# Kernel tuning notes

Hardware: AMD Instinct MI355X
Metric: run time of the kernel (lower is better)

The kernel has to match this reference:

```python
import jax, jax.numpy as jnp
import numpy as np

NUM_HEADS = 16

def setup_inputs() -> dict:
    key = jax.random.key(0)
    ks = jax.random.split(key, 9)
    B, S, D = 2, 2048, 1024
    scale = 1.0 / np.sqrt(D)
    x = jax.random.normal(ks[0], (B, S, D), dtype=jnp.float32)
    def lin(k):
        kw, kb = jax.random.split(k)
        w = jax.random.uniform(kw, (D, D), jnp.float32, -scale, scale)
        b = jax.random.uniform(kb, (D,), jnp.float32, -scale, scale)
        return w, b
    wq, bq = lin(ks[1])
    wk, bk = lin(ks[2])
    wv, bv = lin(ks[3])
    wo, bo = lin(ks[4])
    return {"x": x, "wq": wq, "bq": bq, "wk": wk, "bk": bk,
            "wv": wv, "bv": bv, "wo": wo, "bo": bo}

def reference(x, wq, bq, wk, bk, wv, bv, wo, bo):
    # Prefill path: past_kv=None, use_cache=False, dropout in eval mode (identity).
    B, S, D = x.shape
    H = NUM_HEADS
    Hd = D // H
    # Linear layers: y = x @ W^T + b (torch nn.Linear convention)
    q = (x @ wq.T + bq).reshape(B, S, H, Hd)
    k = (x @ wk.T + bk).reshape(B, S, H, Hd)
    v = (x @ wv.T + bv).reshape(B, S, H, Hd)
    # scores: (B, H, S, S)
    scores = jnp.einsum("bqhd,bkhd->bhqk", q, k) / np.sqrt(Hd).astype(np.float32)
    # causal mask (seq_len > 1 and past_kv is None)
    causal = jnp.tril(jnp.ones((S, S), dtype=bool))
    scores = jnp.where(causal, scores, -jnp.inf)
    probs = jax.nn.softmax(scores, axis=-1)
    attn = jnp.einsum("bhqk,bkhd->bqhd", probs, v).reshape(B, S, D)
    return attn @ wo.T + bo
```

## Files before the change

kernel.cpp:

```cpp
#include <hip/hip_runtime.h>
#include <hip/hip_bf16.h>
#include <math.h>

constexpr int Bt   = 2;
constexpr int Sseq = 2048;
constexpr int Dm   = 1024;
constexpr int Hh   = 16;
constexpr int Mrows = Bt * Sseq;
constexpr int Kd    = 1024;

typedef __attribute__((ext_vector_type(8))) short bf16x8;
typedef __attribute__((ext_vector_type(4))) float f32x4;

__device__ __forceinline__ ushort bfhi(float x) {
    __hip_bfloat16 h = __float2bfloat16(x);
    return *reinterpret_cast<ushort*>(&h);
}
__device__ __forceinline__ float bf2f(ushort u) {
    __hip_bfloat16 h;
    *reinterpret_cast<ushort*>(&h) = u;
    return __bfloat162float(h);
}
__device__ __forceinline__ void split2(float x, ushort& h, ushort& l) {
    h = bfhi(x);
    l = bfhi(x - bf2f(h));
}

template<int MODE>
__global__ __launch_bounds__(256)
void gemm_bf16x2(const float* __restrict__ A,
                 const float* __restrict__ W0, const float* __restrict__ W1,
                 const float* __restrict__ W2,
                 const float* __restrict__ b0, const float* __restrict__ b1,
                 const float* __restrict__ b2,
                 float* __restrict__ Cf,
                 ushort* __restrict__ qk_hi, ushort* __restrict__ qk_lo,
                 ushort* __restrict__ vt_hi, ushort* __restrict__ vt_lo)
{
    __shared__ alignas(16) ushort As[128 * 64];
    __shared__ alignas(16) ushort Bs[128 * 64];

    const int tid = threadIdx.x, lane = tid & 63, w = tid >> 6;

    const int gx = gridDim.x;
    int bid = blockIdx.y * gx + blockIdx.x;
    int cpx = (gx * gridDim.y) >> 3;
    int sb  = (bid & 7) * cpx + (bid >> 3);
    const int m0 = (sb / gx) * 128;
    const int j0 = (sb % gx) * 128;

    const int wsel = j0 >> 10;
    const float* __restrict__ W    = (wsel == 0) ? W0 : ((wsel == 1) ? W1 : W2);
    const float* __restrict__ bias = (wsel == 0) ? b0 : ((wsel == 1) ? b1 : b2);
    const int jj0 = j0 & 1023;

    const int wr = w >> 1, wc = w & 1;
    const int rl = lane & 15, kq = lane >> 4;
    const int sw0 = rl & 7;

    const int srow  = tid >> 1;
    const int khalf = tid & 1;
    const int rsw   = srow & 7;

    const float* ga0 = A + (size_t)(m0  + srow) * Kd + khalf * 16;
    const float* gb0 = W + (size_t)(jj0 + srow) * Kd + khalf * 16;

    f32x4 acc[4][4] = {};
    float av[16], bv[16];

    #pragma unroll
    for (int p = 0; p < 4; ++p) {
        *(float4*)&av[p * 4] = *(const float4*)(ga0 + p * 4);
        *(float4*)&bv[p * 4] = *(const float4*)(gb0 + p * 4);
    }

    for (int k0 = 0; k0 < Kd; k0 += 32) {
        __syncthreads();
        {
            ushort* pa = As + srow * 64;
            ushort* pb = Bs + srow * 64;
            #pragma unroll
            for (int t = 0; t < 2; ++t) {
                bf16x8 hia, loa, hib, lob;
                #pragma unroll
                for (int e = 0; e < 8; ++e) {
                    float xa = av[t * 8 + e], xb = bv[t * 8 + e];
                    ushort ha, la, hb, lb;
                    split2(xa, ha, la); split2(xb, hb, lb);
                    hia[e] = (short)ha; loa[e] = (short)la;
                    hib[e] = (short)hb; lob[e] = (short)lb;
                }
                int s = khalf * 2 + t;
                *(bf16x8*)(pa + ((s    ) ^ rsw) * 8) = hia;
                *(bf16x8*)(pa + ((s + 4) ^ rsw) * 8) = loa;
                *(bf16x8*)(pb + ((s    ) ^ rsw) * 8) = hib;
                *(bf16x8*)(pb + ((s + 4) ^ rsw) * 8) = lob;
            }
        }
        __syncthreads();

        if (k0 + 32 < Kd) {
            #pragma unroll
            for (int p = 0; p < 4; ++p) {
                *(float4*)&av[p * 4] = *(const float4*)(ga0 + k0 + 32 + p * 4);
                *(float4*)&bv[p * 4] = *(const float4*)(gb0 + k0 + 32 + p * 4);
            }
        }

        bf16x8 ah[4], al[4], bh[4], bl[4];
        #pragma unroll
        for (int i = 0; i < 4; ++i) {
            const ushort* pa = As + (wr * 64 + i * 16 + rl) * 64;
            ah[i] = *(const bf16x8*)(pa + ((kq    ) ^ sw0) * 8);
            al[i] = *(const bf16x8*)(pa + ((kq + 4) ^ sw0) * 8);
            const ushort* pb = Bs + (wc * 64 + i * 16 + rl) * 64;
            bh[i] = *(const bf16x8*)(pb + ((kq    ) ^ sw0) * 8);
            bl[i] = *(const bf16x8*)(pb + ((kq + 4) ^ sw0) * 8);
        }
        __builtin_amdgcn_s_setprio(1);
        #pragma unroll
        for (int i = 0; i < 4; ++i)
            #pragma unroll
            for (int j = 0; j < 4; ++j) {
                acc[i][j] = __builtin_amdgcn_mfma_f32_16x16x32_bf16(ah[i], bh[j], acc[i][j], 0, 0, 0);
                acc[i][j] = __builtin_amdgcn_mfma_f32_16x16x32_bf16(ah[i], bl[j], acc[i][j], 0, 0, 0);
                acc[i][j] = __builtin_amdgcn_mfma_f32_16x16x32_bf16(al[i], bh[j], acc[i][j], 0, 0, 0);
            }
        __builtin_amdgcn_s_setprio(0);
    }

    #pragma unroll
    for (int i = 0; i < 4; ++i)
        #pragma unroll
        for (int j = 0; j < 4; ++j) {
            int col = j0 + wc * 64 + j * 16 + rl;
            float bv_ = bias[col & 1023];
            int token0 = m0 + wr * 64 + i * 16 + kq * 4;
            if constexpr (MODE == 1) {
                #pragma unroll
                for (int r = 0; r < 4; ++r)
                    Cf[(size_t)(token0 + r) * 1024 + col] = acc[i][j][r] + bv_;
            } else {
                if (col < 2048) {
                    float scale = (col < 1024) ? 0.125f : 1.0f;
                    #pragma unroll
                    for (int r = 0; r < 4; ++r) {
                        float val = (acc[i][j][r] + bv_) * scale;
                        ushort hs, ls;
                        split2(val, hs, ls);
                        size_t idx = (size_t)(token0 + r) * 2048 + col;
                        qk_hi[idx] = hs;
                        qk_lo[idx] = ls;
                    }
                } else {
                    int cc = col - 2048;
                    int hh = cc >> 6, dd = cc & 63;
                    int bb = token0 >> 11, s0 = token0 & 2047;
                    ushort hs[4], ls[4];
                    #pragma unroll
                    for (int r = 0; r < 4; ++r)
                        split2(acc[i][j][r] + bv_, hs[r], ls[r]);
                    size_t vrow = ((size_t)(bb * 16 + hh) * 64 + dd) * 2048 + s0;
                    *(ushort4*)(vt_hi + vrow) = make_ushort4(hs[0], hs[1], hs[2], hs[3]);
                    *(ushort4*)(vt_lo + vrow) = make_ushort4(ls[0], ls[1], ls[2], ls[3]);
                }
            }
        }
}

__global__ __launch_bounds__(256)
void attn_mfma(const ushort* __restrict__ qk_hi, const ushort* __restrict__ qk_lo,
               const ushort* __restrict__ vt_hi, const ushort* __restrict__ vt_lo,
               float* __restrict__ aout)
{
    __shared__ alignas(16) ushort Kh[4096], Kl[4096], Vh[4096], Vl[4096];
    __shared__ alignas(16) uint   P32[4][2048];

    const int xx = blockIdx.x;
    const int qt = (xx & 1) ? (xx >> 1) : (15 - (xx >> 1));
    const int h  = blockIdx.y, b = blockIdx.z;
    const int q0 = qt * 128;
    const int tid = threadIdx.x, lane = tid & 63, w = tid >> 6;
    const int rl = lane & 15, kq = lane >> 4;

    bf16x8 qfh[2][2], qfl[2][2];
    {
        const size_t qrow = (size_t)(b * Sseq + q0 + w * 32);
        #pragma unroll
        for (int mi = 0; mi < 2; ++mi)
            #pragma unroll
            for (int s = 0; s < 2; ++s) {
                size_t g = (qrow + mi * 16 + rl) * 2048 + h * 64 + s * 32 + kq * 8;
                qfh[mi][s] = *(const bf16x8*)(qk_hi + g);
                qfl[mi][s] = *(const bf16x8*)(qk_lo + g);
            }
    }

    f32x4 accO[2][4] = {};
    float m_i[2][4], l_i[2][4];
    #pragma unroll
    for (int mi = 0; mi < 2; ++mi)
        #pragma unroll
        for (int r = 0; r < 4; ++r) { m_i[mi][r] = -INFINITY; l_i[mi][r] = 0.0f; }

    const int srow = tid >> 2, sc2 = tid & 3;
    const size_t kbase = (size_t)(b * Sseq) * 2048 + 1024 + h * 64 + sc2 * 16;
    const size_t vbase = ((size_t)((b * 16 + h) * 64) + srow) * 2048 + sc2 * 16;
    const int swA = (sc2 * 2 + 0) ^ (srow & 7);
    const int swB = (sc2 * 2 + 1) ^ (srow & 7);

    bf16x8 stg[8];
    auto ISSUE = [&](int kv0) {
        size_t gk = kbase + (size_t)(kv0 + srow) * 2048;
        size_t gv = vbase + kv0;
        stg[0] = *(const bf16x8*)(qk_hi + gk);
        stg[1] = *(const bf16x8*)(qk_hi + gk + 8);
        stg[2] = *(const bf16x8*)(qk_lo + gk);
        stg[3] = *(const bf16x8*)(qk_lo + gk + 8);
        stg[4] = *(const bf16x8*)(vt_hi + gv);
        stg[5] = *(const bf16x8*)(vt_hi + gv + 8);
        stg[6] = *(const bf16x8*)(vt_lo + gv);
        stg[7] = *(const bf16x8*)(vt_lo + gv + 8);
    };

    const int NT = 2 * qt + 2;
    ISSUE(0);

    for (int kt = 0; kt < NT; ++kt) {
        __syncthreads();
        {
            *(bf16x8*)(Kh + srow * 64 + swA * 8) = stg[0];
            *(bf16x8*)(Kh + srow * 64 + swB * 8) = stg[1];
            *(bf16x8*)(Kl + srow * 64 + swA * 8) = stg[2];
            *(bf16x8*)(Kl + srow * 64 + swB * 8) = stg[3];
            *(bf16x8*)(Vh + srow * 64 + swA * 8) = stg[4];
            *(bf16x8*)(Vh + srow * 64 + swB * 8) = stg[5];
            *(bf16x8*)(Vl + srow * 64 + swA * 8) = stg[6];
            *(bf16x8*)(Vl + srow * 64 + swB * 8) = stg[7];
        }
        __syncthreads();

        if (kt + 1 < NT) ISSUE((kt + 1) * 64);

        const int kv0 = kt * 64;

        f32x4 sc[2][4] = {};
        #pragma unroll
        for (int s = 0; s < 2; ++s) {
            bf16x8 kh[4], kl[4];
            #pragma unroll
            for (int n = 0; n < 4; ++n) {
                int row = n * 16 + rl;
                int sw = (s * 4 + kq) ^ (row & 7);
                kh[n] = *(const bf16x8*)(Kh + row * 64 + sw * 8);
                kl[n] = *(const bf16x8*)(Kl + row * 64 + sw * 8);
            }
            __builtin_amdgcn_s_setprio(1);
            #pragma unroll
            for (int mi = 0; mi < 2; ++mi)
                #pragma unroll
                for (int n = 0; n < 4; ++n) {
                    sc[mi][n] = __builtin_amdgcn_mfma_f32_16x16x32_bf16(qfh[mi][s], kh[n], sc[mi][n], 0, 0, 0);
                    sc[mi][n] = __builtin_amdgcn_mfma_f32_16x16x32_bf16(qfh[mi][s], kl[n], sc[mi][n], 0, 0, 0);
                    sc[mi][n] = __builtin_amdgcn_mfma_f32_16x16x32_bf16(qfl[mi][s], kh[n], sc[mi][n], 0, 0, 0);
                }
            __builtin_amdgcn_s_setprio(0);
        }

        if (kt >= 2 * qt) {
            #pragma unroll
            for (int mi = 0; mi < 2; ++mi)
                #pragma unroll
                for (int n = 0; n < 4; ++n)
                    #pragma unroll
                    for (int r = 0; r < 4; ++r)
                        if (kv0 + n * 16 + rl > q0 + w * 32 + mi * 16 + kq * 4 + r)
                            sc[mi][n][r] = -INFINITY;
        }

        float fs[2][4];
        #pragma unroll
        for (int mi = 0; mi < 2; ++mi)
            #pragma unroll
            for (int r = 0; r < 4; ++r) {
                float v = fmaxf(fmaxf(sc[mi][0][r], sc[mi][1][r]),
                                fmaxf(sc[mi][2][r], sc[mi][3][r]));
                v = fmaxf(v, __shfl_xor(v, 1));
                v = fmaxf(v, __shfl_xor(v, 2));
                v = fmaxf(v, __shfl_xor(v, 4));
                v = fmaxf(v, __shfl_xor(v, 8));
                float mnew = fmaxf(m_i[mi][r], v);
                fs[mi][r]  = __expf(m_i[mi][r] - mnew);
                m_i[mi][r] = mnew;
            }

        #pragma unroll
        for (int mi = 0; mi < 2; ++mi)
            #pragma unroll
            for (int r = 0; r < 4; ++r) {
                int q = mi * 16 + kq * 4 + r;
                float sum = 0.0f;
                #pragma unroll
                for (int n = 0; n < 4; ++n) {
                    float p = __expf(sc[mi][n][r] - m_i[mi][r]);
                    sum += p;
                    ushort hs, ls;
                    split2(p, hs, ls);
                    int c = n * 4 + (rl >> 2);
                    P32[w][q * 64 + ((c ^ (q & 7)) << 2) + (rl & 3)] =
                        (uint)hs | ((uint)ls << 16);
                }
                sum += __shfl_xor(sum, 1);
                sum += __shfl_xor(sum, 2);
                sum += __shfl_xor(sum, 4);
                sum += __shfl_xor(sum, 8);
                l_i[mi][r] = l_i[mi][r] * fs[mi][r] + sum;
            }

        #pragma unroll
        for (int mi = 0; mi < 2; ++mi)
            #pragma unroll
            for (int n = 0; n < 4; ++n)
                #pragma unroll
                for (int r = 0; r < 4; ++r)
                    accO[mi][n][r] *= fs[mi][r];

        #pragma unroll
        for (int s2 = 0; s2 < 2; ++s2) {
            bf16x8 vh[4], vl[4];
            #pragma unroll
            for (int n = 0; n < 4; ++n) {
                int row = n * 16 + rl;
                int sw = (s2 * 4 + kq) ^ (row & 7);
                vh[n] = *(const bf16x8*)(Vh + row * 64 + sw * 8);
                vl[n] = *(const bf16x8*)(Vl + row * 64 + sw * 8);
            }
            #pragma unroll
            for (int mi = 0; mi < 2; ++mi) {
                uint u[8];
                #pragma unroll
                for (int cc = 0; cc < 2; ++cc) {
                    int c = s2 * 8 + kq * 2 + cc;
                    const uint* pp = &P32[w][(mi * 16 + rl) * 64 + ((c ^ (rl & 7)) << 2)];
                    uint4 uu = *(const uint4*)pp;
                    u[cc * 4 + 0] = uu.x; u[cc * 4 + 1] = uu.y;
                    u[cc * 4 + 2] = uu.z; u[cc * 4 + 3] = uu.w;
                }
                uint tph[4], tpl[4];
                #pragma unroll
                for (int jw = 0; jw < 4; ++jw) {
                    tph[jw] = (u[2 * jw] & 0xffffu) | (u[2 * jw + 1] << 16);
                    tpl[jw] = (u[2 * jw] >> 16) | (u[2 * jw + 1] & 0xffff0000u);
                }
                bf16x8 ph = *reinterpret_cast<bf16x8*>(tph);
                bf16x8 pl = *reinterpret_cast<bf16x8*>(tpl);
                __builtin_amdgcn_s_setprio(1);
                #pragma unroll
                for (int n = 0; n < 4; ++n) {
                    accO[mi][n] = __builtin_amdgcn_mfma_f32_16x16x32_bf16(ph, vh[n], accO[mi][n], 0, 0, 0);
                    accO[mi][n] = __builtin_amdgcn_mfma_f32_16x16x32_bf16(ph, vl[n], accO[mi][n], 0, 0, 0);
                    accO[mi][n] = __builtin_amdgcn_mfma_f32_16x16x32_bf16(pl, vh[n], accO[mi][n], 0, 0, 0);
                }
                __builtin_amdgcn_s_setprio(0);
            }
        }
    }

    #pragma unroll
    for (int mi = 0; mi < 2; ++mi)
        #pragma unroll
        for (int r = 0; r < 4; ++r) {
            float inv = 1.0f / l_i[mi][r];
            int token = b * Sseq + q0 + w * 32 + mi * 16 + kq * 4 + r;
            #pragma unroll
            for (int n = 0; n < 4; ++n)
                aout[(size_t)token * 1024 + h * 64 + n * 16 + rl] = accO[mi][n][r] * inv;
        }
}

extern "C" void kernel_launch(void* const* d_in, const int* in_sizes, int n_in,
                              void* d_out, int out_size, void* d_ws, size_t ws_size,
                              hipStream_t stream)
{
    const float* x  = (const float*)d_in[0];
    const float* wq = (const float*)d_in[1];
    const float* bq = (const float*)d_in[2];
    const float* wk = (const float*)d_in[3];
    const float* bk = (const float*)d_in[4];
    const float* wv = (const float*)d_in[5];
    const float* bv = (const float*)d_in[6];
    const float* wo = (const float*)d_in[7];
    const float* bo = (const float*)d_in[8];
    float* out = (float*)d_out;

    const size_t NEED = 67108864;
    if (ws_size < NEED) return;

    char* p = (char*)d_ws;
    ushort* qk_hi = (ushort*)(p);
    ushort* qk_lo = (ushort*)(p + 16777216);
    ushort* vt_hi = (ushort*)(p + 33554432);
    ushort* vt_lo = (ushort*)(p + 41943040);
    float*  attn  = (float*) (p + 50331648);

    gemm_bf16x2<0><<<dim3(24, 32), 256, 0, stream>>>(
        x, wq, wk, wv, bq, bk, bv, nullptr, qk_hi, qk_lo, vt_hi, vt_lo);

    attn_mfma<<<dim3(16, Hh, Bt), 256, 0, stream>>>(
        qk_hi, qk_lo, vt_hi, vt_lo, attn);

    gemm_bf16x2<1><<<dim3(8, 32), 256, 0, stream>>>(
        attn, wo, wo, wo, bo, bo, bo, out, nullptr, nullptr, nullptr, nullptr);
}
```

Measured before the change: 465.8 us.

## Rewrite attention with 32x32 MFMA and transposed scores, dropping LDS P staging

The attention kernel switches from 16x16x32 to 32x32x16 bf16 MFMA and computes S^T = K·Q^T, so each lane holds a full query row's scores. Softmax reductions then need only a single cross-half shuffle. P is rearranged into the A-operand layout in registers via lane shuffles, which removes the per-warp LDS P buffer and its writes and reads. The output is written with float4 stores. The cost is higher register pressure from 16-wide accumulators, and there is a risk of layout errors in the shuffle remapping.

After: 429.5 us. -7.8%, faster.

```diff
diff --git a/kernel.cpp b/kernel.cpp
--- a/kernel.cpp
+++ b/kernel.cpp
@@ -9,8 +9,9 @@
 constexpr int Mrows = Bt * Sseq;
 constexpr int Kd    = 1024;
 
-typedef __attribute__((ext_vector_type(8))) short bf16x8;
-typedef __attribute__((ext_vector_type(4))) float f32x4;
+typedef __attribute__((ext_vector_type(8)))  short bf16x8;
+typedef __attribute__((ext_vector_type(4)))  float f32x4;
+typedef __attribute__((ext_vector_type(16))) float f32x16;
 
 __device__ __forceinline__ ushort bfhi(float x) {
     __hip_bfloat16 h = __float2bfloat16(x);
@@ -169,39 +170,33 @@
 }
 
 __global__ __launch_bounds__(256)
-void attn_mfma(const ushort* __restrict__ qk_hi, const ushort* __restrict__ qk_lo,
-               const ushort* __restrict__ vt_hi, const ushort* __restrict__ vt_lo,
-               float* __restrict__ aout)
+void attn_mfma32(const ushort* __restrict__ qk_hi, const ushort* __restrict__ qk_lo,
+                 const ushort* __restrict__ vt_hi, const ushort* __restrict__ vt_lo,
+                 float* __restrict__ aout)
 {
     __shared__ alignas(16) ushort Kh[4096], Kl[4096], Vh[4096], Vl[4096];
-    __shared__ alignas(16) uint   P32[4][2048];
 
     const int xx = blockIdx.x;
     const int qt = (xx & 1) ? (xx >> 1) : (15 - (xx >> 1));
     const int h  = blockIdx.y, b = blockIdx.z;
     const int q0 = qt * 128;
-    const int tid = threadIdx.x, lane = tid & 63, w = tid >> 6;
-    const int rl = lane & 15, kq = lane >> 4;
-
-    bf16x8 qfh[2][2], qfl[2][2];
+    const int tid = threadIdx.x, l = tid & 63, w = tid >> 6;
+    const int lo5 = l & 31, hi = l >> 5;
+
+    bf16x8 qh[4], ql[4];
     {
-        const size_t qrow = (size_t)(b * Sseq + q0 + w * 32);
-        #pragma unroll
-        for (int mi = 0; mi < 2; ++mi)
-            #pragma unroll
-            for (int s = 0; s < 2; ++s) {
-                size_t g = (qrow + mi * 16 + rl) * 2048 + h * 64 + s * 32 + kq * 8;
-                qfh[mi][s] = *(const bf16x8*)(qk_hi + g);
-                qfl[mi][s] = *(const bf16x8*)(qk_lo + g);
-            }
-    }
-
-    f32x4 accO[2][4] = {};
-    float m_i[2][4], l_i[2][4];
-    #pragma unroll
-    for (int mi = 0; mi < 2; ++mi)
-        #pragma unroll
-        for (int r = 0; r < 4; ++r) { m_i[mi][r] = -INFINITY; l_i[mi][r] = 0.0f; }
+        const size_t qrow = (size_t)(b * Sseq + q0 + w * 32 + lo5);
+        #pragma unroll
+        for (int s = 0; s < 4; ++s) {
+            size_t g = qrow * 2048 + h * 64 + s * 16 + hi * 8;
+            qh[s] = *(const bf16x8*)(qk_hi + g);
+            ql[s] = *(const bf16x8*)(qk_lo + g);
+        }
+    }
+
+    f32x16 accO[2] = {};
+    float m_r = -INFINITY, l_r = 0.0f;
+    const int qg = q0 + w * 32 + lo5;
 
     const int srow = tid >> 2, sc2 = tid & 3;
     const size_t kbase = (size_t)(b * Sseq) * 2048 + 1024 + h * 64 + sc2 * 16;
@@ -244,138 +239,114 @@
 
         const int kv0 = kt * 64;
 
-        f32x4 sc[2][4] = {};
-        #pragma unroll
-        for (int s = 0; s < 2; ++s) {
-            bf16x8 kh[4], kl[4];
-            #pragma unroll
-            for (int n = 0; n < 4; ++n) {
-                int row = n * 16 + rl;
-                int sw = (s * 4 + kq) ^ (row & 7);
-                kh[n] = *(const bf16x8*)(Kh + row * 64 + sw * 8);
-                kl[n] = *(const bf16x8*)(Kl + row * 64 + sw * 8);
-            }
+        f32x16 sc[2] = {};
+        #pragma unroll
+        for (int s = 0; s < 4; ++s) {
             __builtin_amdgcn_s_setprio(1);
             #pragma unroll
-            for (int mi = 0; mi < 2; ++mi)
+            for (int n = 0; n < 2; ++n) {
+                int row = n * 32 + lo5;
+                int sl = (s * 2 + hi) ^ (row & 7);
+                bf16x8 kh = *(const bf16x8*)(Kh + row * 64 + sl * 8);
+                bf16x8 kl = *(const bf16x8*)(Kl + row * 64 + sl * 8);
+                sc[n] = __builtin_amdgcn_mfma_f32_32x32x16_bf16(kh, qh[s], sc[n], 0, 0, 0);
+                sc[n] = __builtin_amdgcn_mfma_f32_32x32x16_bf16(kh, ql[s], sc[n], 0, 0, 0);
+                sc[n] = __builtin_amdgcn_mfma_f32_32x32x16_bf16(kl, qh[s], sc[n], 0, 0, 0);
+            }
+            __builtin_amdgcn_s_setprio(0);
+        }
+
+        if (kt >= 2 * qt) {
+            #pragma unroll
+            for (int n = 0; n < 2; ++n)
                 #pragma unroll
-                for (int n = 0; n < 4; ++n) {
-                    sc[mi][n] = __builtin_amdgcn_mfma_f32_16x16x32_bf16(qfh[mi][s], kh[n], sc[mi][n], 0, 0, 0);
-                    sc[mi][n] = __builtin_amdgcn_mfma_f32_16x16x32_bf16(qfh[mi][s], kl[n], sc[mi][n], 0, 0, 0);
-                    sc[mi][n] = __builtin_amdgcn_mfma_f32_16x16x32_bf16(qfl[mi][s], kh[n], sc[mi][n], 0, 0, 0);
+                for (int r = 0; r < 16; ++r) {
+                    int kv = kv0 + n * 32 + ((r & 3) + 8 * (r >> 2) + 4 * hi);
+                    if (kv > qg) sc[n][r] = -INFINITY;
                 }
+        }
+
+        float vmax = -INFINITY;
+        #pragma unroll
+        for (int n = 0; n < 2; ++n)
+            #pragma unroll
+            for (int r = 0; r < 16; ++r)
+                vmax = fmaxf(vmax, sc[n][r]);
+        vmax = fmaxf(vmax, __shfl_xor(vmax, 32));
+        float mnew = fmaxf(m_r, vmax);
+        float fs = __expf(m_r - mnew);
+        m_r = mnew;
+
+        uint phk[2][8], plk[2][8];
+        float sum = 0.0f;
+        #pragma unroll
+        for (int n = 0; n < 2; ++n)
+            #pragma unroll
+            for (int j = 0; j < 8; ++j) {
+                float p0 = __expf(sc[n][2 * j]     - mnew);
+                float p1 = __expf(sc[n][2 * j + 1] - mnew);
+                sum += p0 + p1;
+                ushort h0, l0, h1, l1;
+                split2(p0, h0, l0);
+                split2(p1, h1, l1);
+                phk[n][j] = (uint)h0 | ((uint)h1 << 16);
+                plk[n][j] = (uint)l0 | ((uint)l1 << 16);
+            }
+        sum += __shfl_xor(sum, 32);
+        l_r = l_r * fs + sum;
+
+        #pragma unroll
+        for (int nd = 0; nd < 2; ++nd)
+            #pragma unroll
+            for (int r = 0; r < 16; ++r)
+                accO[nd][r] *= fs;
+
+        #pragma unroll
+        for (int step = 0; step < 4; ++step) {
+            const int n  = step >> 1;
+            const int io = (step & 1) * 4 + hi * 2;
+            const int is = (step & 1) * 4 + (1 - hi) * 2;
+            uint oh0 = phk[n][io], oh1 = phk[n][io + 1];
+            uint ol0 = plk[n][io], ol1 = plk[n][io + 1];
+            uint sh0 = (uint)__shfl_xor((int)phk[n][is],     32);
+            uint sh1 = (uint)__shfl_xor((int)phk[n][is + 1], 32);
+            uint sl0 = (uint)__shfl_xor((int)plk[n][is],     32);
+            uint sl1 = (uint)__shfl_xor((int)plk[n][is + 1], 32);
+            uint fh[4], fl[4];
+            if (hi) { fh[0] = sh0; fh[1] = sh1; fh[2] = oh0; fh[3] = oh1;
+                      fl[0] = sl0; fl[1] = sl1; fl[2] = ol0; fl[3] = ol1; }
+            else    { fh[0] = oh0; fh[1] = oh1; fh[2] = sh0; fh[3] = sh1;
+                      fl[0] = ol0; fl[1] = ol1; fl[2] = sl0; fl[3] = sl1; }
+            bf16x8 ph = *reinterpret_cast<bf16x8*>(fh);
+            bf16x8 pl = *reinterpret_cast<bf16x8*>(fl);
+
+            __builtin_amdgcn_s_setprio(1);
+            #pragma unroll
+            for (int nd = 0; nd < 2; ++nd) {
+                int row = nd * 32 + lo5;
+                int sl_ = (step * 2 + hi) ^ (row & 7);
+                bf16x8 vh = *(const bf16x8*)(Vh + row * 64 + sl_ * 8);
+                bf16x8 vl = *(const bf16x8*)(Vl + row * 64 + sl_ * 8);
+                accO[nd] = __builtin_amdgcn_mfma_f32_32x32x16_bf16(vh, ph, accO[nd], 0, 0, 0);
+                accO[nd] = __builtin_amdgcn_mfma_f32_32x32x16_bf16(vh, pl, accO[nd], 0, 0, 0);
+                accO[nd] = __builtin_amdgcn_mfma_f32_32x32x16_bf16(vl, ph, accO[nd], 0, 0, 0);
+            }
             __builtin_amdgcn_s_setprio(0);
         }
-
-        if (kt >= 2 * qt) {
-            #pragma unroll
-            for (int mi = 0; mi < 2; ++mi)
-                #pragma unroll
-                for (int n = 0; n < 4; ++n)
-                    #pragma unroll
-                    for (int r = 0; r < 4; ++r)
-                        if (kv0 + n * 16 + rl > q0 + w * 32 + mi * 16 + kq * 4 + r)
-                            sc[mi][n][r] = -INFINITY;
-        }
-
-        float fs[2][4];
-        #pragma unroll
-        for (int mi = 0; mi < 2; ++mi)
-            #pragma unroll
-            for (int r = 0; r < 4; ++r) {
-                float v = fmaxf(fmaxf(sc[mi][0][r], sc[mi][1][r]),
-                                fmaxf(sc[mi][2][r], sc[mi][3][r]));
-                v = fmaxf(v, __shfl_xor(v, 1));
-                v = fmaxf(v, __shfl_xor(v, 2));
-                v = fmaxf(v, __shfl_xor(v, 4));
-                v = fmaxf(v, __shfl_xor(v, 8));
-                float mnew = fmaxf(m_i[mi][r], v);
-                fs[mi][r]  = __expf(m_i[mi][r] - mnew);
-                m_i[mi][r] = mnew;
-            }
-
-        #pragma unroll
-        for (int mi = 0; mi < 2; ++mi)
-            #pragma unroll
-            for (int r = 0; r < 4; ++r) {
-                int q = mi * 16 + kq * 4 + r;
-                float sum = 0.0f;
-                #pragma unroll
-                for (int n = 0; n < 4; ++n) {
-                    float p = __expf(sc[mi][n][r] - m_i[mi][r]);
-                    sum += p;
-                    ushort hs, ls;
-                    split2(p, hs, ls);
-                    int c = n * 4 + (rl >> 2);
-                    P32[w][q * 64 + ((c ^ (q & 7)) << 2) + (rl & 3)] =
-                        (uint)hs | ((uint)ls << 16);
-                }
-                sum += __shfl_xor(sum, 1);
-                sum += __shfl_xor(sum, 2);
-                sum += __shfl_xor(sum, 4);
-                sum += __shfl_xor(sum, 8);
-                l_i[mi][r] = l_i[mi][r] * fs[mi][r] + sum;
-            }
-
-        #pragma unroll
-        for (int mi = 0; mi < 2; ++mi)
-            #pragma unroll
-            for (int n = 0; n < 4; ++n)
-                #pragma unroll
-                for (int r = 0; r < 4; ++r)
-                    accO[mi][n][r] *= fs[mi][r];
-
-        #pragma unroll
-        for (int s2 = 0; s2 < 2; ++s2) {
-            bf16x8 vh[4], vl[4];
-            #pragma unroll
-            for (int n = 0; n < 4; ++n) {
-                int row = n * 16 + rl;
-                int sw = (s2 * 4 + kq) ^ (row & 7);
-                vh[n] = *(const bf16x8*)(Vh + row * 64 + sw * 8);
-                vl[n] = *(const bf16x8*)(Vl + row * 64 + sw * 8);
-            }
-            #pragma unroll
-            for (int mi = 0; mi < 2; ++mi) {
-                uint u[8];
-                #pragma unroll
-                for (int cc = 0; cc < 2; ++cc) {
-                    int c = s2 * 8 + kq * 2 + cc;
-                    const uint* pp = &P32[w][(mi * 16 + rl) * 64 + ((c ^ (rl & 7)) << 2)];
-                    uint4 uu = *(const uint4*)pp;
-                    u[cc * 4 + 0] = uu.x; u[cc * 4 + 1] = uu.y;
-                    u[cc * 4 + 2] = uu.z; u[cc * 4 + 3] = uu.w;
-                }
-                uint tph[4], tpl[4];
-                #pragma unroll
-                for (int jw = 0; jw < 4; ++jw) {
-                    tph[jw] = (u[2 * jw] & 0xffffu) | (u[2 * jw + 1] << 16);
-                    tpl[jw] = (u[2 * jw] >> 16) | (u[2 * jw + 1] & 0xffff0000u);
-                }
-                bf16x8 ph = *reinterpret_cast<bf16x8*>(tph);
-                bf16x8 pl = *reinterpret_cast<bf16x8*>(tpl);
-                __builtin_amdgcn_s_setprio(1);
-                #pragma unroll
-                for (int n = 0; n < 4; ++n) {
-                    accO[mi][n] = __builtin_amdgcn_mfma_f32_16x16x32_bf16(ph, vh[n], accO[mi][n], 0, 0, 0);
-                    accO[mi][n] = __builtin_amdgcn_mfma_f32_16x16x32_bf16(ph, vl[n], accO[mi][n], 0, 0, 0);
-                    accO[mi][n] = __builtin_amdgcn_mfma_f32_16x16x32_bf16(pl, vh[n], accO[mi][n], 0, 0, 0);
-                }
-                __builtin_amdgcn_s_setprio(0);
-            }
-        }
-    }
-
-    #pragma unroll
-    for (int mi = 0; mi < 2; ++mi)
-        #pragma unroll
-        for (int r = 0; r < 4; ++r) {
-            float inv = 1.0f / l_i[mi][r];
-            int token = b * Sseq + q0 + w * 32 + mi * 16 + kq * 4 + r;
-            #pragma unroll
-            for (int n = 0; n < 4; ++n)
-                aout[(size_t)token * 1024 + h * 64 + n * 16 + rl] = accO[mi][n][r] * inv;
-        }
+    }
+
+    {
+        float inv = 1.0f / l_r;
+        const size_t token = (size_t)(b * Sseq + q0 + w * 32 + lo5);
+        #pragma unroll
+        for (int nd = 0; nd < 2; ++nd)
+            #pragma unroll
+            for (int rg = 0; rg < 4; ++rg) {
+                float4 o = { accO[nd][4 * rg + 0] * inv, accO[nd][4 * rg + 1] * inv,
+                             accO[nd][4 * rg + 2] * inv, accO[nd][4 * rg + 3] * inv };
+                *(float4*)&aout[token * 1024 + h * 64 + nd * 32 + 8 * rg + 4 * hi] = o;
+            }
+    }
 }
 
 extern "C" void kernel_launch(void* const* d_in, const int* in_sizes, int n_in,
@@ -406,7 +377,7 @@
     gemm_bf16x2<0><<<dim3(24, 32), 256, 0, stream>>>(
         x, wq, wk, wv, bq, bk, bv, nullptr, qk_hi, qk_lo, vt_hi, vt_lo);
 
-    attn_mfma<<<dim3(16, Hh, Bt), 256, 0, stream>>>(
+    attn_mfma32<<<dim3(16, Hh, Bt), 256, 0, stream>>>(
         qk_hi, qk_lo, vt_hi, vt_lo, attn);
 
     gemm_bf16x2<1><<<dim3(8, 32), 256, 0, stream>>>(
```
